# Performance work log

Hardware: AMD Instinct MI355X
Metric: run time of the kernel (lower is better)

The kernel has to match this reference:

```python
import jax, jax.numpy as jnp
import numpy as np

N_EXPERTS = 64
N_ACTIVATED = 8
BALANCE_LOSS_ALPHA = 1e-4
EPS = 1e-9


def setup_inputs() -> dict:
    key = jax.random.key(0)
    k1, k2 = jax.random.split(key)
    T, D = 16384, 2048
    x = jax.random.normal(k1, (T, D), dtype=jnp.float32)
    # nn.Linear(hidden_dim, n_experts, bias=False) weight: (n_experts, hidden_dim)
    W_gate = jax.random.normal(k2, (N_EXPERTS, D), dtype=jnp.float32) * (1.0 / np.sqrt(D))
    expert_bias = jnp.zeros((N_EXPERTS,), dtype=jnp.float32)
    return {"x": x, "W_gate": W_gate, "expert_bias": expert_bias}


def reference(x, W_gate, expert_bias):
    T = x.shape[0]
    # sigmoid gating: (T, E)
    affinity = jax.nn.sigmoid(jnp.einsum('td,ed->te', x, W_gate))
    # bias only steers selection (aux-loss-free balancing), not gate values
    routing_scores = affinity + expert_bias[None, :]
    _, topk_indices = jax.lax.top_k(routing_scores, N_ACTIVATED)  # (T, K)
    gate_values = jnp.take_along_axis(affinity, topk_indices, axis=1)  # (T, K)
    gate_values = gate_values / (gate_values.sum(axis=-1, keepdims=True) + EPS)
    # balance loss: per-expert selection frequency f times mean normalized affinity P
    counts = jnp.zeros((N_EXPERTS,), dtype=affinity.dtype).at[topk_indices.reshape(-1)].add(1.0)
    f = counts * (N_EXPERTS / (N_ACTIVATED * T))
    affinity_norm = affinity / (affinity.sum(axis=-1, keepdims=True) + EPS)
    P = affinity_norm.mean(axis=0)
    balance_loss = BALANCE_LOSS_ALPHA * jnp.sum(f * P)
    return gate_values, topk_indices, balance_loss
```

## Files before the change

kernel.cpp:

```cpp
#include <hip/hip_runtime.h>
#include <math.h>

#define T_TOK 16384
#define DIM   2048
#define NE    64
#define NACT  8
#define ALPHA 1e-4f
#define EPSV  1e-9f
#define TAU   2.5e-4f

#define WPITCH 520

typedef __attribute__((ext_vector_type(8))) short bf16x8;
typedef __attribute__((ext_vector_type(4))) float f32x4;

__device__ inline unsigned short bf16_rne(float f) {
    unsigned b = __float_as_uint(f);
    unsigned r = b + 0x7FFFu + ((b >> 16) & 1u);
    return (unsigned short)(r >> 16);
}

__global__ __launch_bounds__(256) void zero_k(float* __restrict__ Aout,
                                              float* __restrict__ gz) {
    const int i = blockIdx.x * 256 + threadIdx.x;
    ((float4*)Aout)[i] = (float4){0.f, 0.f, 0.f, 0.f};
    if (blockIdx.x == 0 && threadIdx.x < 130) gz[threadIdx.x] = 0.0f;
}

__global__ __launch_bounds__(1024) void gemm_k(
        const float* __restrict__ x,
        const float* __restrict__ W,
        float* __restrict__ Aout) {
    __shared__ __align__(16) unsigned short Whs[NE * WPITCH];
    __shared__ __align__(16) unsigned short Wls[NE * WPITCH];

    const int tid = threadIdx.x;
    const int kq  = blockIdx.x & 3;
    const int tg  = blockIdx.x >> 2;
    const int tokBase = tg * 256;
    const int kb  = kq * 512;

    {
        const int e = tid >> 4;
        const int c = tid & 15;
        const float* wr = W + (size_t)e * DIM + kb + c * 32;
        unsigned short* dh = &Whs[e * WPITCH + c * 32];
        unsigned short* dl = &Wls[e * WPITCH + c * 32];
#pragma unroll
        for (int m = 0; m < 8; ++m) {
            const float4 v = *(const float4*)(wr + m * 4);
            const float f[4] = {v.x, v.y, v.z, v.w};
            unsigned short hp[4], lp[4];
#pragma unroll
            for (int u = 0; u < 4; ++u) {
                const unsigned bb = __float_as_uint(f[u]);
                const unsigned hb = bb & 0xFFFF0000u;
                hp[u] = (unsigned short)(hb >> 16);
                lp[u] = bf16_rne(f[u] - __uint_as_float(hb));
            }
            const int dpos = (m & 3) * 8 + (m >> 2) * 4;
            *(ushort4*)(dh + dpos) = *(const ushort4*)hp;
            *(ushort4*)(dl + dpos) = *(const ushort4*)lp;
        }
    }
    __syncthreads();

    const int wv   = tid >> 6;
    const int lane = tid & 63;
    const int c15  = lane & 15;
    const int q    = lane >> 4;

    const float* xp = x + (size_t)(tokBase + wv * 16 + c15) * DIM + kb + q * 4;
    const unsigned short* whB = &Whs[c15 * WPITCH + q * 8];
    const unsigned short* wlB = &Wls[c15 * WPITCH + q * 8];

    f32x4 acc[4];
#pragma unroll
    for (int j = 0; j < 4; ++j) acc[j] = (f32x4){0.f, 0.f, 0.f, 0.f};

    float4 ra[2][2];
    bf16x8 rh[2][4], rl[2][4];

#define LOADSTEP(s, st) {                                                 \
        const float* xpc = xp + 32 * (st);                                \
        ra[s][0] = *(const float4*)xpc;                                   \
        ra[s][1] = *(const float4*)(xpc + 16);                            \
        _Pragma("unroll")                                                 \
        for (int j = 0; j < 4; ++j) {                                     \
            rh[s][j] = *(const bf16x8*)(whB + j * 16 * WPITCH + (st) * 32); \
            rl[s][j] = *(const bf16x8*)(wlB + j * 16 * WPITCH + (st) * 32); \
        }                                                                 \
    }

#define COMPSTEP(s) {                                                     \
        bf16x8 ah, al;                                                    \
        {                                                                 \
            float f[8] = {ra[s][0].x, ra[s][0].y, ra[s][0].z, ra[s][0].w, \
                          ra[s][1].x, ra[s][1].y, ra[s][1].z, ra[s][1].w};\
            _Pragma("unroll")                                             \
            for (int i = 0; i < 8; ++i) {                                 \
                const unsigned bb = __float_as_uint(f[i]);                \
                const unsigned hb = bb & 0xFFFF0000u;                     \
                ah[i] = (short)(hb >> 16);                                \
                al[i] = (short)bf16_rne(f[i] - __uint_as_float(hb));      \
            }                                                             \
        }                                                                 \
        _Pragma("unroll")                                                 \
        for (int j = 0; j < 4; ++j) {                                     \
            acc[j] = __builtin_amdgcn_mfma_f32_16x16x32_bf16(ah, rh[s][j], acc[j], 0, 0, 0); \
            acc[j] = __builtin_amdgcn_mfma_f32_16x16x32_bf16(ah, rl[s][j], acc[j], 0, 0, 0); \
            acc[j] = __builtin_amdgcn_mfma_f32_16x16x32_bf16(al, rh[s][j], acc[j], 0, 0, 0); \
        }                                                                 \
    }

    LOADSTEP(0, 0);
    LOADSTEP(1, 1);
#pragma unroll
    for (int c = 0; c < 16; c += 2) {
        COMPSTEP(0);
        if (c + 2 < 16) LOADSTEP(0, c + 2);
        COMPSTEP(1);
        if (c + 3 < 16) LOADSTEP(1, c + 3);
    }
#undef LOADSTEP
#undef COMPSTEP

    const int trow = tokBase + wv * 16 + q * 4;
#pragma unroll
    for (int j = 0; j < 4; ++j)
#pragma unroll
        for (int r = 0; r < 4; ++r)
            atomicAdd(&Aout[(size_t)(trow + r) * NE + 16 * j + c15], acc[j][r]);
}

__global__ __launch_bounds__(256) void gate_k(
        const float* __restrict__ Aout,
        const float* __restrict__ bias,
        float* __restrict__ gates,
        float* __restrict__ idxf,
        float* __restrict__ gP,
        float* __restrict__ gC,
        int*   __restrict__ cntp,
        int*   __restrict__ list) {
    __shared__ __align__(16) float aff[16 * 68];
    __shared__ __align__(16) float sS[4][64];
    __shared__ __align__(16) float bS[4][64];
    __shared__ __align__(16) float bA[4][64];
    __shared__ float Pl[NE];
    __shared__ float Cl[NE];

    const int tid  = threadIdx.x;
    const int wv   = tid >> 6;
    const int lane = tid & 63;
    const int tokBase = blockIdx.x * 16;

    if (tid < NE) { Pl[tid] = 0.0f; Cl[tid] = 0.0f; }

    {
        const int t  = tid >> 4;
        const int e0 = (tid & 15) * 4;
        const float4 lg = *(const float4*)(Aout + (size_t)(tokBase + t) * NE + e0);
        float4 af;
        af.x = 1.0f / (1.0f + expf(-lg.x));
        af.y = 1.0f / (1.0f + expf(-lg.y));
        af.z = 1.0f / (1.0f + expf(-lg.z));
        af.w = 1.0f / (1.0f + expf(-lg.w));
        *(float4*)&aff[t * 68 + e0] = af;
    }
    __syncthreads();

    const float b = bias[lane];
    float pacc = 0.0f;
    float cacc = 0.0f;

    for (int it = 0; it < 4; ++it) {
        const int tl = wv * 4 + it;
        const int gt = tokBase + tl;
        const float a = aff[tl * 68 + lane];

        float rs = a;
#pragma unroll
        for (int off = 32; off; off >>= 1) rs += __shfl_xor(rs, off, 64);
        pacc += a / (rs + EPSV);

        const float s = a + b;
        sS[wv][lane] = s;
        __syncthreads();

        int rank = 0;
#pragma unroll
        for (int j4 = 0; j4 < 16; ++j4) {
            const float4 sv = *(const float4*)&sS[wv][j4 * 4];
            rank += (sv.x > s || (sv.x == s && (j4 * 4 + 0) < lane));
            rank += (sv.y > s || (sv.y == s && (j4 * 4 + 1) < lane));
            rank += (sv.z > s || (sv.z == s && (j4 * 4 + 2) < lane));
            rank += (sv.w > s || (sv.w == s && (j4 * 4 + 3) < lane));
        }
        bS[wv][rank] = s;
        bA[wv][rank] = a;
        __syncthreads();

        const float4 p0 = *(const float4*)&bS[wv][0];
        const float4 p1 = *(const float4*)&bS[wv][4];
        const float v8v = bS[wv][8];
        float gmin = p0.x - p0.y;
        gmin = fminf(gmin, p0.y - p0.z);
        gmin = fminf(gmin, p0.z - p0.w);
        gmin = fminf(gmin, p0.w - p1.x);
        gmin = fminf(gmin, p1.x - p1.y);
        gmin = fminf(gmin, p1.y - p1.z);
        gmin = fminf(gmin, p1.z - p1.w);
        gmin = fminf(gmin, p1.w - v8v);
        const bool marked = (gmin < TAU);

        const float4 a0 = *(const float4*)&bA[wv][0];
        const float4 a1 = *(const float4*)&bA[wv][4];
        const float gsum = ((((((a0.x + a0.y) + a0.z) + a0.w) + a1.x) + a1.y) + a1.z) + a1.w;
        const float inv = 1.0f / (gsum + EPSV);

        if (rank < NACT) {
            gates[(size_t)gt * NACT + rank] = a * inv;
            idxf [(size_t)gt * NACT + rank] = (float)lane;
            if (!marked) cacc += 1.0f;
        }
        if (lane == 0 && marked) {
            const int slot = atomicAdd(cntp, 1);
            list[slot] = gt;
        }
        __syncthreads();
    }

    atomicAdd(&Pl[lane], pacc);
    atomicAdd(&Cl[lane], cacc);
    __syncthreads();
    if (tid < NE) {
        atomicAdd(&gP[tid], Pl[tid]);
        atomicAdd(&gC[tid], Cl[tid]);
    }
}

__global__ __launch_bounds__(64) void fix_k(
        const float* __restrict__ x,
        const float* __restrict__ Wg,
        const float* __restrict__ bias,
        const float* __restrict__ Aout,
        float* __restrict__ gates,
        float* __restrict__ idxf,
        const float* __restrict__ gP,
        float* __restrict__ gC,
        const int* __restrict__ cntp,
        int*   __restrict__ done,
        const int* __restrict__ list,
        float* __restrict__ lossOut) {
    __shared__ __align__(16) float  sS[64];
    __shared__ __align__(16) float  bS[64];
    __shared__ __align__(16) int    bI[64];
    __shared__ __align__(16) double dS[64];
    __shared__ __align__(16) double dR[64];

    const int lane = threadIdx.x;
    const int cnt = *cntp;
    float cacc = 0.0f;

    for (int idx = blockIdx.x; idx < cnt; idx += gridDim.x) {
        const int t = list[idx];
        const float lg  = Aout[(size_t)t * NE + lane];
        const float a32 = 1.0f / (1.0f + expf(-lg));
        const float bl  = bias[lane];
        const float s32 = a32 + bl;

        const float* xr = x + (size_t)t * DIM;
        float4 xv[8];
#pragma unroll
        for (int m = 0; m < 8; ++m) xv[m] = *(const float4*)(xr + 4 * lane + 256 * m);

        sS[lane] = s32;
        __syncthreads();
        int rank = 0;
#pragma unroll
        for (int j4 = 0; j4 < 16; ++j4) {
            const float4 sv = *(const float4*)&sS[j4 * 4];
            rank += (sv.x > s32 || (sv.x == s32 && (j4 * 4 + 0) < lane));
            rank += (sv.y > s32 || (sv.y == s32 && (j4 * 4 + 1) < lane));
            rank += (sv.z > s32 || (sv.z == s32 && (j4 * 4 + 2) < lane));
            rank += (sv.w > s32 || (sv.w == s32 && (j4 * 4 + 3) < lane));
        }
        bS[rank] = s32;
        bI[rank] = lane;
        __syncthreads();

        float vr[16];
        int   ir[16];
#pragma unroll
        for (int k4 = 0; k4 < 4; ++k4) {
            const float4 vv = *(const float4*)&bS[k4 * 4];
            const int4   ii = *(const int4*)&bI[k4 * 4];
            vr[k4 * 4 + 0] = vv.x; vr[k4 * 4 + 1] = vv.y;
            vr[k4 * 4 + 2] = vv.z; vr[k4 * 4 + 3] = vv.w;
            ir[k4 * 4 + 0] = ii.x; ir[k4 * 4 + 1] = ii.y;
            ir[k4 * 4 + 2] = ii.z; ir[k4 * 4 + 3] = ii.w;
        }
        bool needs[16];
#pragma unroll
        for (int k = 0; k < 16; ++k) needs[k] = false;
#pragma unroll
        for (int k = 1; k <= 8; ++k)
            if (vr[k - 1] - vr[k] < TAU) { needs[k - 1] = true; needs[k] = true; }
#pragma unroll
        for (int k = 9; k < 16; ++k)
            if (needs[k - 1] && (vr[k - 1] - vr[k] < TAU)) needs[k] = true;

        unsigned long long mb = 0ull;
#pragma unroll
        for (int k = 0; k < 16; ++k)
            if (needs[k]) mb |= (1ull << ir[k]);

        double ad = (double)a32;
        while (mb) {
            const int e0 = __ffsll(mb) - 1;
            mb &= mb - 1;
            int e1 = -1;
            if (mb) { e1 = __ffsll(mb) - 1; mb &= mb - 1; }
            const float* wr0 = Wg + (size_t)e0 * DIM;
            const float* wr1 = Wg + (size_t)((e1 >= 0) ? e1 : e0) * DIM;
            float4 w0[8], w1[8];
#pragma unroll
            for (int m = 0; m < 8; ++m) {
                w0[m] = *(const float4*)(wr0 + 4 * lane + 256 * m);
                w1[m] = *(const float4*)(wr1 + 4 * lane + 256 * m);
            }
            double z0 = 0.0, z1 = 0.0;
#pragma unroll
            for (int m = 0; m < 8; ++m) {
                z0 = fma((double)xv[m].x, (double)w0[m].x, z0);
                z0 = fma((double)xv[m].y, (double)w0[m].y, z0);
                z0 = fma((double)xv[m].z, (double)w0[m].z, z0);
                z0 = fma((double)xv[m].w, (double)w0[m].w, z0);
                z1 = fma((double)xv[m].x, (double)w1[m].x, z1);
                z1 = fma((double)xv[m].y, (double)w1[m].y, z1);
                z1 = fma((double)xv[m].z, (double)w1[m].z, z1);
                z1 = fma((double)xv[m].w, (double)w1[m].w, z1);
            }
#pragma unroll
            for (int off = 32; off; off >>= 1) {
                z0 += __shfl_xor(z0, off, 64);
                z1 += __shfl_xor(z1, off, 64);
            }
            const double af0 = 1.0 / (1.0 + exp(-z0));
            if (lane == e0) ad = af0;
            if (e1 >= 0) {
                const double af1 = 1.0 / (1.0 + exp(-z1));
                if (lane == e1) ad = af1;
            }
        }

        const double sd = ad + (double)bl;
        dS[lane] = sd;
        __syncthreads();
        int r2 = 0;
#pragma unroll
        for (int j2 = 0; j2 < 32; ++j2) {
            const double2 dv = *(const double2*)&dS[j2 * 2];
            r2 += (dv.x > sd || (dv.x == sd && (2 * j2 + 0) < lane));
            r2 += (dv.y > sd || (dv.y == sd && (2 * j2 + 1) < lane));
        }
        dR[r2] = ad;
        __syncthreads();
        const double2 g0 = *(const double2*)&dR[0];
        const double2 g1 = *(const double2*)&dR[2];
        const double2 g2 = *(const double2*)&dR[4];
        const double2 g3 = *(const double2*)&dR[6];
        const double gsum = ((((((g0.x + g0.y) + g1.x) + g1.y) + g2.x) + g2.y) + g3.x) + g3.y;
        const double inv = 1.0 / (gsum + (double)EPSV);

        if (r2 < NACT) {
            gates[(size_t)t * NACT + r2] = (float)(ad * inv);
            idxf [(size_t)t * NACT + r2] = (float)lane;
            cacc += 1.0f;
        }
        __syncthreads();
    }

    atomicAdd(&gC[lane], cacc);
    __threadfence();
    int tk = 0;
    if (lane == 0) tk = atomicAdd(done, 1);
    tk = __shfl(tk, 0, 64);
    if (tk == (int)gridDim.x - 1) {
        __threadfence();
        const float f = gC[lane] * ((float)NE / (float)(NACT * T_TOK));
        const float P = gP[lane] / (float)T_TOK;
        float v = f * P;
#pragma unroll
        for (int off = 32; off; off >>= 1) v += __shfl_xor(v, off, 64);
        if (lane == 0) lossOut[0] = ALPHA * v;
    }
}

extern "C" void kernel_launch(void* const* d_in, const int* in_sizes, int n_in,
                              void* d_out, int out_size, void* d_ws, size_t ws_size,
                              hipStream_t stream) {
    const float* x    = (const float*)d_in[0];
    const float* Wg   = (const float*)d_in[1];
    const float* bias = (const float*)d_in[2];
    float* out = (float*)d_out;
    float* gates = out;
    float* idxf  = out + (size_t)T_TOK * NACT;
    float* loss  = out + 2 * (size_t)T_TOK * NACT;

    float* Aout = (float*)d_ws;
    float* gP   = Aout + (size_t)T_TOK * NE;
    float* gC   = gP + NE;
    int*   cntp = (int*)(gC + NE);
    int*   done = cntp + 1;
    int*   list = done + 1;

    zero_k<<<1024, 256, 0, stream>>>(Aout, gP);
    gemm_k<<<256, 1024, 0, stream>>>(x, Wg, Aout);
    gate_k<<<T_TOK / 16, 256, 0, stream>>>(Aout, bias, gates, idxf,
                                           gP, gC, cntp, list);
    fix_k<<<2048, 64, 0, stream>>>(x, Wg, bias, Aout, gates, idxf,
                                   gP, gC, cntp, done, list, loss);
}
```

Before: 328.6 us.

## Fuse gate GEMM with gating, drop split-K atomics, pre-split W in prep kernel

Replaces the zero/split-K GEMM/gate kernel trio with a weight-prep kernel and one fused kernel. The prep kernel converts W once into bf16 hi/lo parts laid out in MFMA fragment order. The fused kernel lets each wave cover the full 2048-wide K loop for 16 tokens, reading W fragments straight from global/L2. It then does the sigmoid and top-k from shared memory, with no atomics, no zeroing pass, and no separate Aout read-back. The cost is fewer blocks (256 blocks of 256 threads) and longer per-wave K loops, which reduces parallelism and latency hiding compared with the 1024-thread split-K design.

```diff
diff --git a/kernel.cpp b/kernel.cpp
--- a/kernel.cpp
+++ b/kernel.cpp
@@ -9,8 +9,6 @@
 #define EPSV  1e-9f
 #define TAU   2.5e-4f
 
-#define WPITCH 520
-
 typedef __attribute__((ext_vector_type(8))) short bf16x8;
 typedef __attribute__((ext_vector_type(4))) float f32x4;
 
@@ -20,59 +18,74 @@
     return (unsigned short)(r >> 16);
 }
 
-__global__ __launch_bounds__(256) void zero_k(float* __restrict__ Aout,
-                                              float* __restrict__ gz) {
-    const int i = blockIdx.x * 256 + threadIdx.x;
-    ((float4*)Aout)[i] = (float4){0.f, 0.f, 0.f, 0.f};
-    if (blockIdx.x == 0 && threadIdx.x < 130) gz[threadIdx.x] = 0.0f;
+__global__ __launch_bounds__(256) void prep_k(
+        const float* __restrict__ W,
+        unsigned short* __restrict__ Wfh,
+        unsigned short* __restrict__ Wfl,
+        float* __restrict__ gz) {
+    const int gid = blockIdx.x * 256 + threadIdx.x;
+    const int lane = gid & 63;
+    const int j    = (gid >> 6) & 3;
+    const int st   = gid >> 8;
+    const int c15  = lane & 15;
+    const int q    = lane >> 4;
+    const int e    = 16 * j + c15;
+    const int k0   = st * 32 + q * 4;
+
+    const float* wr = W + (size_t)e * DIM + k0;
+    const float4 v0 = *(const float4*)(wr);
+    const float4 v1 = *(const float4*)(wr + 16);
+    const float f[8] = {v0.x, v0.y, v0.z, v0.w, v1.x, v1.y, v1.z, v1.w};
+
+    unsigned short hp[8], lp[8];
+#pragma unroll
+    for (int i = 0; i < 8; ++i) {
+        const unsigned bb = __float_as_uint(f[i]);
+        const unsigned hb = bb & 0xFFFF0000u;
+        hp[i] = (unsigned short)(hb >> 16);
+        lp[i] = bf16_rne(f[i] - __uint_as_float(hb));
+    }
+    unsigned short* dh = Wfh + (size_t)gid * 8;
+    unsigned short* dl = Wfl + (size_t)gid * 8;
+    *(ushort4*)(dh)     = *(const ushort4*)(hp);
+    *(ushort4*)(dh + 4) = *(const ushort4*)(hp + 4);
+    *(ushort4*)(dl)     = *(const ushort4*)(lp);
+    *(ushort4*)(dl + 4) = *(const ushort4*)(lp + 4);
+
+    if (gid < 130) gz[gid] = 0.0f;
 }
 
-__global__ __launch_bounds__(1024) void gemm_k(
+__global__ __launch_bounds__(256) void main_k(
         const float* __restrict__ x,
-        const float* __restrict__ W,
-        float* __restrict__ Aout) {
-    __shared__ __align__(16) unsigned short Whs[NE * WPITCH];
-    __shared__ __align__(16) unsigned short Wls[NE * WPITCH];
-
-    const int tid = threadIdx.x;
-    const int kq  = blockIdx.x & 3;
-    const int tg  = blockIdx.x >> 2;
-    const int tokBase = tg * 256;
-    const int kb  = kq * 512;
-
-    {
-        const int e = tid >> 4;
-        const int c = tid & 15;
-        const float* wr = W + (size_t)e * DIM + kb + c * 32;
-        unsigned short* dh = &Whs[e * WPITCH + c * 32];
-        unsigned short* dl = &Wls[e * WPITCH + c * 32];
-#pragma unroll
-        for (int m = 0; m < 8; ++m) {
-            const float4 v = *(const float4*)(wr + m * 4);
-            const float f[4] = {v.x, v.y, v.z, v.w};
-            unsigned short hp[4], lp[4];
-#pragma unroll
-            for (int u = 0; u < 4; ++u) {
-                const unsigned bb = __float_as_uint(f[u]);
-                const unsigned hb = bb & 0xFFFF0000u;
-                hp[u] = (unsigned short)(hb >> 16);
-                lp[u] = bf16_rne(f[u] - __uint_as_float(hb));
-            }
-            const int dpos = (m & 3) * 8 + (m >> 2) * 4;
-            *(ushort4*)(dh + dpos) = *(const ushort4*)hp;
-            *(ushort4*)(dl + dpos) = *(const ushort4*)lp;
-        }
-    }
-    __syncthreads();
-
+        const unsigned short* __restrict__ Wfh,
+        const unsigned short* __restrict__ Wfl,
+        const float* __restrict__ bias,
+        float* __restrict__ Aout,
+        float* __restrict__ gates,
+        float* __restrict__ idxf,
+        float* __restrict__ gP,
+        float* __restrict__ gC,
+        int*   __restrict__ cntp,
+        int*   __restrict__ list) {
+    __shared__ __align__(16) float aff[4][16 * 68];
+    __shared__ __align__(16) float sS[4][64];
+    __shared__ __align__(16) float bS[4][64];
+    __shared__ __align__(16) float bA[4][64];
+    __shared__ float Pl[NE];
+    __shared__ float Cl[NE];
+
+    const int tid  = threadIdx.x;
     const int wv   = tid >> 6;
     const int lane = tid & 63;
     const int c15  = lane & 15;
     const int q    = lane >> 4;
-
-    const float* xp = x + (size_t)(tokBase + wv * 16 + c15) * DIM + kb + q * 4;
-    const unsigned short* whB = &Whs[c15 * WPITCH + q * 8];
-    const unsigned short* wlB = &Wls[c15 * WPITCH + q * 8];
+    const int tw   = blockIdx.x * 64 + wv * 16;
+
+    if (tid < NE) { Pl[tid] = 0.0f; Cl[tid] = 0.0f; }
+
+    const float* xc = x + (size_t)(tw + c15) * DIM + q * 4;
+    const unsigned short* whc = Wfh + (size_t)lane * 8;
+    const unsigned short* wlc = Wfl + (size_t)lane * 8;
 
     f32x4 acc[4];
 #pragma unroll
@@ -81,14 +94,13 @@
     float4 ra[2][2];
     bf16x8 rh[2][4], rl[2][4];
 
-#define LOADSTEP(s, st) {                                                 \
-        const float* xpc = xp + 32 * (st);                                \
-        ra[s][0] = *(const float4*)xpc;                                   \
-        ra[s][1] = *(const float4*)(xpc + 16);                            \
+#define LOADSTEP(s) {                                                     \
+        ra[s][0] = *(const float4*)(xc + (s) * 32);                       \
+        ra[s][1] = *(const float4*)(xc + (s) * 32 + 16);                  \
         _Pragma("unroll")                                                 \
         for (int j = 0; j < 4; ++j) {                                     \
-            rh[s][j] = *(const bf16x8*)(whB + j * 16 * WPITCH + (st) * 32); \
-            rl[s][j] = *(const bf16x8*)(wlB + j * 16 * WPITCH + (st) * 32); \
+            rh[s][j] = *(const bf16x8*)(whc + (s) * 2048 + j * 512);      \
+            rl[s][j] = *(const bf16x8*)(wlc + (s) * 2048 + j * 512);      \
         }                                                                 \
     }
 
@@ -113,70 +125,39 @@
         }                                                                 \
     }
 
-    LOADSTEP(0, 0);
-    LOADSTEP(1, 1);
-#pragma unroll
-    for (int c = 0; c < 16; c += 2) {
+    LOADSTEP(0);
+    LOADSTEP(1);
+#pragma unroll 3
+    for (int p = 0; p < 31; ++p) {
         COMPSTEP(0);
-        if (c + 2 < 16) LOADSTEP(0, c + 2);
+        xc  += 64;
+        whc += 4096;
+        wlc += 4096;
+        LOADSTEP(0);
         COMPSTEP(1);
-        if (c + 3 < 16) LOADSTEP(1, c + 3);
-    }
+        LOADSTEP(1);
+    }
+    COMPSTEP(0);
+    COMPSTEP(1);
 #undef LOADSTEP
 #undef COMPSTEP
 
-    const int trow = tokBase + wv * 16 + q * 4;
 #pragma unroll
     for (int j = 0; j < 4; ++j)
 #pragma unroll
         for (int r = 0; r < 4; ++r)
-            atomicAdd(&Aout[(size_t)(trow + r) * NE + 16 * j + c15], acc[j][r]);
-}
-
-__global__ __launch_bounds__(256) void gate_k(
-        const float* __restrict__ Aout,
-        const float* __restrict__ bias,
-        float* __restrict__ gates,
-        float* __restrict__ idxf,
-        float* __restrict__ gP,
-        float* __restrict__ gC,
-        int*   __restrict__ cntp,
-        int*   __restrict__ list) {
-    __shared__ __align__(16) float aff[16 * 68];
-    __shared__ __align__(16) float sS[4][64];
-    __shared__ __align__(16) float bS[4][64];
-    __shared__ __align__(16) float bA[4][64];
-    __shared__ float Pl[NE];
-    __shared__ float Cl[NE];
-
-    const int tid  = threadIdx.x;
-    const int wv   = tid >> 6;
-    const int lane = tid & 63;
-    const int tokBase = blockIdx.x * 16;
-
-    if (tid < NE) { Pl[tid] = 0.0f; Cl[tid] = 0.0f; }
-
-    {
-        const int t  = tid >> 4;
-        const int e0 = (tid & 15) * 4;
-        const float4 lg = *(const float4*)(Aout + (size_t)(tokBase + t) * NE + e0);
-        float4 af;
-        af.x = 1.0f / (1.0f + expf(-lg.x));
-        af.y = 1.0f / (1.0f + expf(-lg.y));
-        af.z = 1.0f / (1.0f + expf(-lg.z));
-        af.w = 1.0f / (1.0f + expf(-lg.w));
-        *(float4*)&aff[t * 68 + e0] = af;
-    }
+            aff[wv][(q * 4 + r) * 68 + 16 * j + c15] = acc[j][r];
     __syncthreads();
 
     const float b = bias[lane];
     float pacc = 0.0f;
     float cacc = 0.0f;
 
-    for (int it = 0; it < 4; ++it) {
-        const int tl = wv * 4 + it;
-        const int gt = tokBase + tl;
-        const float a = aff[tl * 68 + lane];
+    for (int t = 0; t < 16; ++t) {
+        const int gt = tw + t;
+        const float lg = aff[wv][t * 68 + lane];
+        Aout[(size_t)gt * NE + lane] = lg;
+        const float a = 1.0f / (1.0f + expf(-lg));
 
         float rs = a;
 #pragma unroll
@@ -409,16 +390,17 @@
     float* loss  = out + 2 * (size_t)T_TOK * NACT;
 
     float* Aout = (float*)d_ws;
-    float* gP   = Aout + (size_t)T_TOK * NE;
+    unsigned short* Wfh = (unsigned short*)((char*)d_ws + (4u << 20));
+    unsigned short* Wfl = (unsigned short*)((char*)d_ws + (4u << 20) + (256u << 10));
+    float* gP   = (float*)((char*)d_ws + (4u << 20) + (512u << 10));
     float* gC   = gP + NE;
     int*   cntp = (int*)(gC + NE);
     int*   done = cntp + 1;
     int*   list = done + 1;
 
-    zero_k<<<1024, 256, 0, stream>>>(Aout, gP);
-    gemm_k<<<256, 1024, 0, stream>>>(x, Wg, Aout);
-    gate_k<<<T_TOK / 16, 256, 0, stream>>>(Aout, bias, gates, idxf,
-                                           gP, gC, cntp, list);
+    prep_k<<<64, 256, 0, stream>>>(Wg, Wfh, Wfl, gP);
+    main_k<<<256, 256, 0, stream>>>(x, Wfh, Wfl, bias, Aout, gates, idxf,
+                                    gP, gC, cntp, list);
     fix_k<<<2048, 64, 0, stream>>>(x, Wg, bias, Aout, gates, idxf,
                                    gP, gC, cntp, done, list, loss);
 }
```

After: 352.3 us. +7.2%, slower.
